# Optimization experiments

Measured on AMD Instinct MI355X. Metric: run time of the kernel, lower is better.

## Reference

```python
import jax, jax.numpy as jnp
import numpy as np

N_PTS = 100000
C_IN, C_OUT, K = 16, 32, 3
B, D, H, W = 2, 32, 128, 128


def setup_inputs() -> dict:
    key = jax.random.key(0)
    kf, kw, kb, kz, ky, kx = jax.random.split(key, 6)
    features = jax.random.normal(kf, (N_PTS, C_IN), dtype=jnp.float32)
    coords = jnp.stack([
        jax.random.randint(kb, (N_PTS,), 0, B),
        jax.random.randint(kz, (N_PTS,), 0, D),
        jax.random.randint(ky, (N_PTS,), 0, H),
        jax.random.randint(kx, (N_PTS,), 0, W),
    ], axis=1).astype(jnp.int32)
    weight = jax.random.normal(kw, (K ** 3, C_IN, C_OUT), dtype=jnp.float32) * 0.01
    bias = jnp.zeros((C_OUT,), dtype=jnp.float32)
    return {"features": features, "coords": coords, "weight": weight, "bias": bias,
            "batch_size": B, "d_sp": D, "h_sp": H, "w_sp": W}


def reference(features, coords, weight, bias, batch_size, d_sp, h_sp, w_sp):
    # Scatter sparse voxel features into dense grid (B, C_in, D, H, W).
    n, c_in = features.shape
    c_out = weight.shape[2]
    k = K
    b, z, y, x = coords[:, 0], coords[:, 1], coords[:, 2], coords[:, 3]
    dense = jnp.zeros((batch_size, c_in, d_sp, h_sp, w_sp), dtype=features.dtype)
    dense = dense.at[b, :, z, y, x].set(features)  # (N,) advanced idx -> rows of (N, C_in)
    # Conv3d: torch copies weight.view(C_out, C_in, k, k, k) -> OIDHW kernel.
    kernel = weight.reshape(c_out, c_in, k, k, k)
    out = jax.lax.conv_general_dilated(
        dense, kernel,
        window_strides=(1, 1, 1),
        padding=[(1, 1), (1, 1), (1, 1)],
        dimension_numbers=("NCDHW", "OIDHW", "NCDHW"))
    out = jax.nn.relu(out + bias[None, :, None, None, None])
    # Dense equivalent of the torch nonzero-gather (which has data-dependent
    # shape): return the full dense activated grid (B, C_out, D, H, W).
    return out
```

## Files before the change

kernel.cpp:

```cpp
#include <hip/hip_runtime.h>

#define CIN   16
#define COUT  32
#define BATCH 2
#define DSP   32
#define HSP   128
#define WSP   128
#define NVOX  (BATCH*DSP*HSP*WSP)

#define TZ 4
#define TY 4
#define TX 32
#define NTZ 8
#define NTY 32
#define NTX 4
#define NTILES (BATCH*NTZ*NTY*NTX)
#define PZ 6
#define PYY 6
#define PXX 34
#define PVOX (PZ*PYY*PXX)
#define HALFU (PVOX*8)
#define NPAIR 14
#define NWREP ((NPAIR*2*64*8 + 255)/256)

typedef __bf16 bf16x8 __attribute__((ext_vector_type(8)));
typedef float  f32x4  __attribute__((ext_vector_type(4)));

__global__ void k_prep(const int4* __restrict__ coords, int n, int nbDedup,
                       int* __restrict__ map,
                       const float* __restrict__ w, __bf16* __restrict__ wpack) {
    int bb = blockIdx.x;
    if (bb < nbDedup) {
        int p = bb * 256 + threadIdx.x;
        if (p >= n) return;
        int4 c = coords[p];
        int vox = ((c.x*DSP + c.y)*HSP + c.z)*WSP + c.w;
        atomicMax(&map[vox], p);
    } else {
        int i = (bb - nbDedup) * 256 + threadIdx.x;
        if (i >= NPAIR*2*64*8) return;
        int j = i & 7, l = (i>>3) & 63, h = (i>>9) & 1, p = i >> 10;
        int tap = 2*p + ((l>>4)>>1);
        int co  = h*16 + (l & 15);
        int ci  = ((l>>4)&1)*8 + j;
        float v = (tap < 27) ? w[(co*CIN + ci)*27 + tap] : 0.0f;
        wpack[i] = (__bf16)v;
    }
}

__global__ void k_scatter(const int4* __restrict__ coords, const int* __restrict__ map,
                          const float* __restrict__ feat, __bf16* __restrict__ dense,
                          int n) {
    int p = blockIdx.x * 256 + threadIdx.x;
    if (p >= n) return;
    int4 c = coords[p];
    int vox = ((c.x*DSP + c.y)*HSP + c.z)*WSP + c.w;
    if (map[vox] != p) return;
    const float4* fp = (const float4*)(feat + (size_t)p*CIN);
    float4 f0 = fp[0], f1 = fp[1], f2 = fp[2], f3 = fp[3];
    bf16x8 lo = { (__bf16)f0.x,(__bf16)f0.y,(__bf16)f0.z,(__bf16)f0.w,
                  (__bf16)f1.x,(__bf16)f1.y,(__bf16)f1.z,(__bf16)f1.w };
    bf16x8 hi = { (__bf16)f2.x,(__bf16)f2.y,(__bf16)f2.z,(__bf16)f2.w,
                  (__bf16)f3.x,(__bf16)f3.y,(__bf16)f3.z,(__bf16)f3.w };
    __bf16* d = dense + (size_t)vox*CIN;
    *(bf16x8*)d       = lo;
    *(bf16x8*)(d + 8) = hi;
}

__global__ __launch_bounds__(256, 4) void k_conv(
    const __bf16* __restrict__ dense, const __bf16* __restrict__ wpack,
    const float* __restrict__ bias, float* __restrict__ out)
{
    __shared__ __align__(16) ushort patch[2*HALFU];

    int tile = blockIdx.x;
    int txi = tile & 3;
    int tyi = (tile >> 2) & 31;
    int tzi = (tile >> 7) & 7;
    int b   = tile >> 10;
    int z0 = tzi*TZ, y0 = tyi*TY, x0 = txi*TX;

    int tid  = threadIdx.x;
    int lane = tid & 63, wave = tid >> 6;
    int lx16  = lane & 15;
    int lhalf = (lane >> 4) & 1;
    int ltp   = (lane >> 4) >> 1;

    int voff[NPAIR];
    #pragma unroll
    for (int p = 0; p < NPAIR; ++p) {
        int tap = 2*p + ltp; if (tap > 26) tap = 26;
        int kd = tap/9, kh = (tap/3)%3, kw = tap%3;
        voff[p] = (kd*PYY + kh)*PXX + kw;
    }
    float bv0 = bias[lx16], bv1 = bias[16 + lx16];

    for (int u = tid; u < 2*PVOX; u += 256) {
        int v  = u >> 1, h = u & 1;
        int pz = v / (PYY*PXX);
        int rem = v - pz*(PYY*PXX);
        int py = rem / PXX;
        int px = rem - py*PXX;
        int gz = z0 - 1 + pz, gy = y0 - 1 + py, gx = x0 - 1 + px;
        uint4 val = make_uint4(0,0,0,0);
        if ((unsigned)gz < DSP && (unsigned)gy < HSP && (unsigned)gx < WSP) {
            size_t vox = (((size_t)b*DSP + gz)*HSP + gy)*WSP + gx;
            val = ((const uint4*)(dense + vox*CIN))[h];
        }
        *(uint4*)(patch + h*HALFU + v*8) = val;
    }
    __syncthreads();

    f32x4 acc[8][2];
    #pragma unroll
    for (int gi = 0; gi < 8; ++gi) {
        acc[gi][0] = (f32x4){0.f,0.f,0.f,0.f};
        acc[gi][1] = (f32x4){0.f,0.f,0.f,0.f};
    }
    const ushort* pb = patch + lhalf*HALFU + ((wave*PYY)*PXX + lx16)*8;
    bf16x8 w0 = *(const bf16x8*)(wpack + (size_t)(0*64 + lane)*8);
    bf16x8 w1 = *(const bf16x8*)(wpack + (size_t)(1*64 + lane)*8);
    #pragma unroll
    for (int p = 0; p < NPAIR; ++p) {
        int pn = (p + 1 < NPAIR) ? p + 1 : 0;
        bf16x8 nw0 = *(const bf16x8*)(wpack + (size_t)((pn*2+0)*64 + lane)*8);
        bf16x8 nw1 = *(const bf16x8*)(wpack + (size_t)((pn*2+1)*64 + lane)*8);
        const ushort* pa = pb + voff[p]*8;
        #pragma unroll
        for (int gi = 0; gi < 8; ++gi) {
            int y = gi >> 1, xg = gi & 1;
            bf16x8 a = *(const bf16x8*)(pa + (y*PXX + xg*16)*8);
            acc[gi][0] = __builtin_amdgcn_mfma_f32_16x16x32_bf16(a, w0, acc[gi][0], 0,0,0);
            acc[gi][1] = __builtin_amdgcn_mfma_f32_16x16x32_bf16(a, w1, acc[gi][1], 0,0,0);
        }
        w0 = nw0; w1 = nw1;
    }

    #pragma unroll
    for (int gi = 0; gi < 8; ++gi) {
        int y = gi >> 1, xg = gi & 1;
        int gz = z0 + wave, gy = y0 + y, gx = x0 + xg*16 + ((lane >> 4) << 2);
        f32x4 o0, o1;
        o0[0] = fmaxf(acc[gi][0][0]+bv0, 0.f); o0[1] = fmaxf(acc[gi][0][1]+bv0, 0.f);
        o0[2] = fmaxf(acc[gi][0][2]+bv0, 0.f); o0[3] = fmaxf(acc[gi][0][3]+bv0, 0.f);
        o1[0] = fmaxf(acc[gi][1][0]+bv1, 0.f); o1[1] = fmaxf(acc[gi][1][1]+bv1, 0.f);
        o1[2] = fmaxf(acc[gi][1][2]+bv1, 0.f); o1[3] = fmaxf(acc[gi][1][3]+bv1, 0.f);
        size_t base0 = ((((size_t)b*COUT + lx16)*DSP + gz)*HSP + gy)*WSP + gx;
        size_t base1 = base0 + (size_t)16*DSP*HSP*WSP;
        __builtin_nontemporal_store(o0, (f32x4*)(out + base0));
        __builtin_nontemporal_store(o1, (f32x4*)(out + base1));
    }
}

extern "C" void kernel_launch(void* const* d_in, const int* in_sizes, int n_in,
                              void* d_out, int out_size, void* d_ws, size_t ws_size,
                              hipStream_t stream) {
    const float* feat   = (const float*)d_in[0];
    const int4*  coords = (const int4*)d_in[1];
    const float* weight = (const float*)d_in[2];
    const float* bias   = (const float*)d_in[3];
    float* out = (float*)d_out;
    int n = in_sizes[0] / CIN;

    int*    map   = (int*)d_ws;
    __bf16* dense = (__bf16*)(map + NVOX);
    __bf16* wpack = dense + (size_t)NVOX*CIN;

    hipMemsetAsync(map, 0xFF, (size_t)NVOX*sizeof(int), stream);
    hipMemsetAsync(dense, 0, (size_t)NVOX*CIN*sizeof(__bf16), stream);

    int nb = (n + 255) / 256;
    k_prep   <<<nb + NWREP, 256, 0, stream>>>(coords, n, nb, map, weight, wpack);
    k_scatter<<<nb, 256, 0, stream>>>(coords, map, feat, dense, n);
    k_conv   <<<NTILES, 256, 0, stream>>>(dense, wpack, bias, out);
}
```

Measured before the change: 80.74 us.

## Pad dense grid and read conv operands directly from global memory, dropping LDS patch

The dense bf16 grid is stored with a one-voxel zero halo, so the conv kernel can read its MFMA A operands straight from global or L2 using fixed tap offsets. This removes the shared-memory patch staging, its bounds checks and the block barrier. Tiles are remapped across blocks (strided by 8), likely to spread neighbouring tiles across XCDs or caches, and the tap loop is only partially unrolled. In exchange every block re-reads overlapping halo data through the cache hierarchy instead of reusing it from LDS, and the memset grows slightly because of the padding.

Result: slower. 118.8 us (+47.2%).

```diff
diff --git a/kernel.cpp b/kernel.cpp
--- a/kernel.cpp
+++ b/kernel.cpp
@@ -8,18 +8,16 @@
 #define WSP   128
 #define NVOX  (BATCH*DSP*HSP*WSP)
 
+#define DP (DSP+2)
+#define HP (HSP+2)
+#define WP (WSP+2)
+#define ZSTR (HP*WP)
+#define NVOXP (BATCH*DP*HP*WP)
+
 #define TZ 4
 #define TY 4
 #define TX 32
-#define NTZ 8
-#define NTY 32
-#define NTX 4
-#define NTILES (BATCH*NTZ*NTY*NTX)
-#define PZ 6
-#define PYY 6
-#define PXX 34
-#define PVOX (PZ*PYY*PXX)
-#define HALFU (PVOX*8)
+#define NTILES 2048
 #define NPAIR 14
 #define NWREP ((NPAIR*2*64*8 + 255)/256)
 
@@ -62,7 +60,8 @@
                   (__bf16)f1.x,(__bf16)f1.y,(__bf16)f1.z,(__bf16)f1.w };
     bf16x8 hi = { (__bf16)f2.x,(__bf16)f2.y,(__bf16)f2.z,(__bf16)f2.w,
                   (__bf16)f3.x,(__bf16)f3.y,(__bf16)f3.z,(__bf16)f3.w };
-    __bf16* d = dense + (size_t)vox*CIN;
+    size_t voxp = (((size_t)c.x*DP + (c.y+1))*HP + (c.z+1))*WP + (c.w+1);
+    __bf16* d = dense + voxp*CIN;
     *(bf16x8*)d       = lo;
     *(bf16x8*)(d + 8) = hi;
 }
@@ -71,9 +70,8 @@
     const __bf16* __restrict__ dense, const __bf16* __restrict__ wpack,
     const float* __restrict__ bias, float* __restrict__ out)
 {
-    __shared__ __align__(16) ushort patch[2*HALFU];
-
-    int tile = blockIdx.x;
+    int bid  = blockIdx.x;
+    int tile = (bid & 7) * (NTILES/8) + (bid >> 3);
     int txi = tile & 3;
     int tyi = (tile >> 2) & 31;
     int tzi = (tile >> 7) & 7;
@@ -86,30 +84,17 @@
     int lhalf = (lane >> 4) & 1;
     int ltp   = (lane >> 4) >> 1;
 
-    int voff[NPAIR];
+    int woff[NPAIR];
     #pragma unroll
     for (int p = 0; p < NPAIR; ++p) {
         int tap = 2*p + ltp; if (tap > 26) tap = 26;
         int kd = tap/9, kh = (tap/3)%3, kw = tap%3;
-        voff[p] = (kd*PYY + kh)*PXX + kw;
+        woff[p] = (kd-1)*ZSTR + (kh-1)*WP + (kw-1);
     }
     float bv0 = bias[lx16], bv1 = bias[16 + lx16];
 
-    for (int u = tid; u < 2*PVOX; u += 256) {
-        int v  = u >> 1, h = u & 1;
-        int pz = v / (PYY*PXX);
-        int rem = v - pz*(PYY*PXX);
-        int py = rem / PXX;
-        int px = rem - py*PXX;
-        int gz = z0 - 1 + pz, gy = y0 - 1 + py, gx = x0 - 1 + px;
-        uint4 val = make_uint4(0,0,0,0);
-        if ((unsigned)gz < DSP && (unsigned)gy < HSP && (unsigned)gx < WSP) {
-            size_t vox = (((size_t)b*DSP + gz)*HSP + gy)*WSP + gx;
-            val = ((const uint4*)(dense + vox*CIN))[h];
-        }
-        *(uint4*)(patch + h*HALFU + v*8) = val;
-    }
-    __syncthreads();
+    size_t vbase = (((size_t)b*DP + (z0 + wave + 1))*HP + (y0 + 1))*WP + (x0 + lx16 + 1);
+    const __bf16* pb = dense + vbase*CIN + lhalf*8;
 
     f32x4 acc[8][2];
     #pragma unroll
@@ -117,19 +102,18 @@
         acc[gi][0] = (f32x4){0.f,0.f,0.f,0.f};
         acc[gi][1] = (f32x4){0.f,0.f,0.f,0.f};
     }
-    const ushort* pb = patch + lhalf*HALFU + ((wave*PYY)*PXX + lx16)*8;
+
     bf16x8 w0 = *(const bf16x8*)(wpack + (size_t)(0*64 + lane)*8);
     bf16x8 w1 = *(const bf16x8*)(wpack + (size_t)(1*64 + lane)*8);
-    #pragma unroll
+    #pragma unroll 2
     for (int p = 0; p < NPAIR; ++p) {
         int pn = (p + 1 < NPAIR) ? p + 1 : 0;
         bf16x8 nw0 = *(const bf16x8*)(wpack + (size_t)((pn*2+0)*64 + lane)*8);
         bf16x8 nw1 = *(const bf16x8*)(wpack + (size_t)((pn*2+1)*64 + lane)*8);
-        const ushort* pa = pb + voff[p]*8;
+        const __bf16* pa = pb + (ptrdiff_t)woff[p]*CIN;
         #pragma unroll
         for (int gi = 0; gi < 8; ++gi) {
-            int y = gi >> 1, xg = gi & 1;
-            bf16x8 a = *(const bf16x8*)(pa + (y*PXX + xg*16)*8);
+            bf16x8 a = *(const bf16x8*)(pa + ((gi>>1)*WP + (gi&1)*16)*CIN);
             acc[gi][0] = __builtin_amdgcn_mfma_f32_16x16x32_bf16(a, w0, acc[gi][0], 0,0,0);
             acc[gi][1] = __builtin_amdgcn_mfma_f32_16x16x32_bf16(a, w1, acc[gi][1], 0,0,0);
         }
@@ -164,10 +148,10 @@
 
     int*    map   = (int*)d_ws;
     __bf16* dense = (__bf16*)(map + NVOX);
-    __bf16* wpack = dense + (size_t)NVOX*CIN;
+    __bf16* wpack = dense + (size_t)NVOXP*CIN;
 
     hipMemsetAsync(map, 0xFF, (size_t)NVOX*sizeof(int), stream);
-    hipMemsetAsync(dense, 0, (size_t)NVOX*CIN*sizeof(__bf16), stream);
+    hipMemsetAsync(dense, 0, (size_t)NVOXP*CIN*sizeof(__bf16), stream);
 
     int nb = (n + 255) / 256;
     k_prep   <<<nb + NWREP, 256, 0, stream>>>(coords, n, nb, map, weight, wpack);
```
